# Performance work log

Measured on AMD Instinct MI355X. Metric: run time of the kernel, lower is better.

The kernel has to match this reference:

```python
import jax, jax.numpy as jnp
from jax import lax
import numpy as np

# Config mirroring init_kwargs
B, N, PD = 4, 16384, 3
PROJ = 64                 # projection_channel
M1, K1, C1 = 2048, 32, 128  # level-1 SA: fps points, neighbors, out channel
M2, K2, C2 = 512, 32, 256   # level-2 SA
DH, DO = 512, 256           # dense hidden / out (dense_channels)


def fps(pts, M):
    """Farthest point sampling. pts: [N,3] -> indices [M] (starts at point 0)."""
    n = pts.shape[0]
    def step(carry, _):
        dmin, last = carry
        d = jnp.sum((pts - pts[last]) ** 2, axis=-1)   # dist to newest center
        dmin = jnp.minimum(dmin, d)
        nxt = jnp.argmax(dmin).astype(jnp.int32)
        return (dmin, nxt), last
    init = (jnp.full((n,), 1e10, pts.dtype), jnp.int32(0))
    _, idxs = lax.scan(step, init, None, length=M)
    return idxs


def sa_level(pts, feats, M, K, Wa, ba, Wb, bb):
    """PointNet++ set abstraction: FPS + kNN (xyz space) + grouped MLP + max."""
    idx = jax.vmap(lambda p: fps(p, M))(pts)                       # [B,M]
    centers = jnp.take_along_axis(pts, idx[:, :, None], axis=1)    # [B,M,3]
    d = jnp.sum((centers[:, :, None, :] - pts[:, None, :, :]) ** 2, -1)  # [B,M,N]
    _, nidx = lax.top_k(-d, K)                                      # [B,M,K]
    gather = jax.vmap(lambda a, i: a[i])
    rel = gather(pts, nidx) - centers[:, :, None, :]                # [B,M,K,3]
    nf = gather(feats, nidx)                                        # [B,M,K,C]
    g = jnp.concatenate([rel, nf], axis=-1)                         # use_xyz=True
    h = jax.nn.relu(g @ Wa + ba)
    h = jax.nn.relu(h @ Wb + bb)
    return centers, jnp.max(h, axis=2)                              # [B,M,Cout]


def setup_inputs() -> dict:
    key = jax.random.key(0)
    ks = jax.random.split(key, 12)
    w = lambda k, shape, s: jax.random.normal(k, shape, jnp.float32) * s
    z = lambda c: jnp.zeros((c,), jnp.float32)
    return {
        "xyz": jax.random.normal(ks[0], (B, N, PD), jnp.float32),
        "Wp": w(ks[1], (PD, PROJ), 0.3), "bp": z(PROJ),
        "W1a": w(ks[2], (PROJ + 3, C1), 0.1), "b1a": z(C1),
        "W1b": w(ks[3], (C1, C1), 0.08), "b1b": z(C1),
        "W2a": w(ks[4], (C1 + 3, C2), 0.08), "b2a": z(C2),
        "W2b": w(ks[5], (C2, C2), 0.06), "b2b": z(C2),
        "Wd1": w(ks[6], (2 * C2, DH), 0.05), "bd1": z(DH),
        "Wd2": w(ks[7], (DH, DO), 0.05), "bd2": z(DO),
    }


def reference(xyz, Wp, bp, W1a, b1a, W1b, b1b, W2a, b2a, W2b, b2b,
              Wd1, bd1, Wd2, bd2):
    feats = xyz @ Wp + bp            # point_proj: [B,N,PROJ]
    pts = xyz[..., :3]
    pts, feats = sa_level(pts, feats, M1, K1, W1a, b1a, W1b, b1b)
    pts, feats = sa_level(pts, feats, M2, K2, W2a, b2a, W2b, b2b)
    # global max + avg pool (adaptive_max/avg_pool1d to 1), concat -> [B,2*C2]
    g = jnp.concatenate([jnp.max(feats, axis=1), jnp.mean(feats, axis=1)], -1)
    h = jax.nn.relu(g @ Wd1 + bd1)   # DenseBlock w/ activation
    return h @ Wd2 + bd2             # last block: no activation (last_activation=False)
```

## Files before the change

### kernel.cpp

```cpp
#include <hip/hip_runtime.h>

#define B_    4
#define N1_   16384
#define M1_   2048
#define M2_   512
#define KNN_  32
#define PROJ_ 64
#define C1_   128
#define C2_   256
#define PROJ_BLKS_ ((B_ * N1_ * PROJ_) / 512)
#define KNN_BLKS_  ((M1_ / 64) * (B_ * 64))

__device__ __forceinline__ float sqdist_exact(float px, float py, float pz,
                                              float cx, float cy, float cz) {
    float dx = __fsub_rn(px, cx);
    float dy = __fsub_rn(py, cy);
    float dz = __fsub_rn(pz, cz);
    return __fadd_rn(__fadd_rn(__fmul_rn(dx, dx), __fmul_rn(dy, dy)), __fmul_rn(dz, dz));
}

typedef float v2f __attribute__((ext_vector_type(2)));

template<int CTRL, int RM>
__device__ __forceinline__ unsigned long long dpp_umax64(unsigned long long pk) {
    unsigned lo = (unsigned)__builtin_amdgcn_update_dpp(
        0, (int)(unsigned)pk, CTRL, RM, 0xf, true);
    unsigned hi = (unsigned)__builtin_amdgcn_update_dpp(
        0, (int)(unsigned)(pk >> 32), CTRL, RM, 0xf, true);
    unsigned long long o = ((unsigned long long)hi << 32) | (unsigned long long)lo;
    return (o > pk) ? o : pk;
}

__device__ __forceinline__ unsigned long long wave_max_key(unsigned long long pk) {
    pk = dpp_umax64<0x111, 0xf>(pk);
    pk = dpp_umax64<0x112, 0xf>(pk);
    pk = dpp_umax64<0x114, 0xf>(pk);
    pk = dpp_umax64<0x118, 0xf>(pk);
    pk = dpp_umax64<0x142, 0xa>(pk);
    pk = dpp_umax64<0x143, 0xc>(pk);
    return pk;
}

__device__ __forceinline__ unsigned reduce8_widx(const unsigned long long* wk,
                                                 int lane) {
    unsigned long long k8 = wk[lane & 7];
    k8 = dpp_umax64<0x111, 0xf>(k8);
    k8 = dpp_umax64<0x112, 0xf>(k8);
    k8 = dpp_umax64<0x114, 0xf>(k8);
    unsigned lo = (unsigned)__builtin_amdgcn_readlane((int)(unsigned)k8, 7);
    return ~lo;
}

__device__ __forceinline__ unsigned reduce2_widx(const unsigned long long* wk,
                                                 int lane) {
    unsigned long long k2 = wk[lane & 1];
    k2 = dpp_umax64<0x111, 0xf>(k2);
    unsigned lo = (unsigned)__builtin_amdgcn_readlane((int)(unsigned)k2, 1);
    return ~lo;
}

template<int N>
__device__ void knn_body512(const float* __restrict__ P,
                            float cx, float cy, float cz,
                            int* __restrict__ out, char* arena) {
    constexpr int K = KNN_;
    constexpr int CAP = 224;
    const int t = threadIdx.x;
    const int lane = t & 63;
    const int w = t >> 6;

    int*      hist = (int*)arena;
    unsigned* eqk  = (unsigned*)(arena + 8192);
    int*      eqi  = (int*)(arena + 8192 + 896);
    int*      wsum = (int*)(arena + 8192 + 1792);
    int*      ctrl = (int*)(arena + 8192 + 1824);

    unsigned prefix = 0; int pbits = 0;
    unsigned Tlo = 0; unsigned long long Thi = 0x100000000ull;
    int L = 0, target = K, Cbin = N;

    for (int round = 0; round < 3; ++round) {
        const int bits  = (round < 2) ? 11 : 10;
        const int nbins = 1 << bits;
        const int shift = 32 - pbits - bits;
        for (int i = t; i < nbins; i += 512) hist[i] = 0;
        __syncthreads();
        for (int j = t; j < N; j += 512) {
            float d = sqdist_exact(P[j * 3], P[j * 3 + 1], P[j * 3 + 2], cx, cy, cz);
            unsigned key = __float_as_uint(d);
            if (key >= Tlo && (unsigned long long)key < Thi)
                atomicAdd(&hist[(key >> shift) & (nbins - 1)], 1);
        }
        __syncthreads();
        const int per = nbins / 512;
        int s = 0;
        for (int i = 0; i < per; ++i) s += hist[t * per + i];
        int cum = s;
        for (int off = 1; off < 64; off <<= 1) {
            int o = __shfl_up(cum, off);
            if (lane >= off) cum += o;
        }
        if (lane == 63) wsum[w] = cum;
        __syncthreads();
        int wpre = 0;
        for (int i = 0; i < w; ++i) wpre += wsum[i];
        cum += wpre;
        const int cumex = cum - s;
        if ((cumex < target) && (cum >= target)) {
            int acc = cumex;
            for (int i = 0; i < per; ++i) {
                int h = hist[t * per + i];
                if (acc + h >= target) { ctrl[2] = t * per + i; ctrl[3] = acc; ctrl[4] = h; break; }
                acc += h;
            }
        }
        __syncthreads();
        const int binsel = ctrl[2];
        const int Ladd   = ctrl[3];
        const int bincnt = ctrl[4];
        L += Ladd;
        target -= Ladd;
        prefix = (prefix << bits) | (unsigned)binsel;
        pbits += bits;
        Tlo = prefix << (32 - pbits);
        Thi = ((unsigned long long)prefix + 1ull) << (32 - pbits);
        Cbin = bincnt;
        __syncthreads();
        if (Cbin <= CAP) break;
    }

    if (t == 0) { ctrl[0] = 0; ctrl[1] = 0; }
    __syncthreads();

    if (Cbin <= CAP) {
        for (int j = t; j < N; j += 512) {
            float d = sqdist_exact(P[j * 3], P[j * 3 + 1], P[j * 3 + 2], cx, cy, cz);
            unsigned key = __float_as_uint(d);
            if (key < Tlo) {
                int p = atomicAdd(&ctrl[0], 1);
                out[p] = j;
            } else if ((unsigned long long)key < Thi) {
                int p = atomicAdd(&ctrl[1], 1);
                eqk[p] = key; eqi[p] = j;
            }
        }
        __syncthreads();
        const int E = ctrl[1];
        for (int e = t; e < E; e += 512) {
            unsigned ke = eqk[e]; int ie = eqi[e];
            int rank = 0;
            for (int f = 0; f < E; ++f) {
                unsigned kf = eqk[f]; int jf = eqi[f];
                rank += (kf < ke || (kf == ke && jf < ie)) ? 1 : 0;
            }
            if (rank < target) out[L + rank] = ie;
        }
    } else {
        if (t < 64) {
            int cnt = 0;
            for (int jb = 0; jb < N; jb += 64) {
                int j = jb + lane;
                float d = sqdist_exact(P[j * 3], P[j * 3 + 1], P[j * 3 + 2], cx, cy, cz);
                unsigned key = __float_as_uint(d);
                if (key < Tlo) {
                    int p = atomicAdd(&ctrl[0], 1);
                    out[p] = j;
                }
                bool eq = (key == Tlo);
                unsigned long long mb = __ballot(eq);
                int below = __popcll(mb & ((1ull << lane) - 1ull));
                if (eq && (cnt + below) < target) out[L + cnt + below] = j;
                cnt += (int)__popcll(mb);
            }
        }
    }
}

__global__ __attribute__((amdgpu_flat_work_group_size(512, 512)))
__attribute__((amdgpu_waves_per_eu(2, 2)))
void mega1_kernel(const float* __restrict__ xyz,
                  const float* __restrict__ Wp, const float* __restrict__ bp,
                  float* __restrict__ feats0, float* __restrict__ centers1,
                  int* __restrict__ nidx1, unsigned* __restrict__ prog) {
#pragma clang fp contract(off)
    __shared__ alignas(16) char arena[24832];
    asm volatile("" ::: "v255");
    const int bid = blockIdx.x;
    const int t = threadIdx.x;

    if (bid >= B_ + PROJ_BLKS_) {
        const int k = bid - (B_ + PROJ_BLKS_);
        const int c = k >> 8;
        const int b = (k >> 6) & 3;
        const int m = c * 64 + (k & 63);
        if (t == 0) {
            while (__hip_atomic_load(&prog[b * 16], __ATOMIC_RELAXED,
                                     __HIP_MEMORY_SCOPE_AGENT) <= (unsigned)c)
                __builtin_amdgcn_s_sleep(16);
        }
        __syncthreads();
        const unsigned* cw = (const unsigned*)(centers1 + ((size_t)b * M1_ + m) * 3);
        float cx = __uint_as_float(__hip_atomic_load(cw + 0, __ATOMIC_RELAXED, __HIP_MEMORY_SCOPE_AGENT));
        float cy = __uint_as_float(__hip_atomic_load(cw + 1, __ATOMIC_RELAXED, __HIP_MEMORY_SCOPE_AGENT));
        float cz = __uint_as_float(__hip_atomic_load(cw + 2, __ATOMIC_RELAXED, __HIP_MEMORY_SCOPE_AGENT));
        knn_body512<N1_>(xyz + (size_t)b * N1_ * 3, cx, cy, cz,
                         nidx1 + ((size_t)b * M1_ + m) * KNN_, arena);
        return;
    }
    if (bid >= B_) {
        int tid = (bid - B_) * 512 + t;
        int cc = tid & (PROJ_ - 1);
        int pn = tid >> 6;
        const float* p = xyz + (size_t)pn * 3;
        float acc = p[0] * Wp[0 * PROJ_ + cc];
        acc = __fmaf_rn(p[1], Wp[1 * PROJ_ + cc], acc);
        acc = __fmaf_rn(p[2], Wp[2 * PROJ_ + cc], acc);
        feats0[tid] = acc + bp[cc];
        return;
    }
    constexpr int NT = 512;
    constexpr int NW = NT / 64;
    constexpr int NP1 = (N1_ / NT) / 2;
    const int b = bid;
    const int w = t >> 6;
    const int lane = t & 63;
    const float* P = xyz + (size_t)b * N1_ * 3;
    float* C1 = centers1 + (size_t)b * M1_ * 3;

    unsigned long long (*wkey)[NW] = (unsigned long long(*)[NW])arena;
    float* cb1 = (float*)(arena + 128);

    v2f px2[NP1], py2[NP1], pz2[NP1];
    float dmin[2 * NP1];
#pragma unroll
    for (int p = 0; p < NP1; ++p) {
        const int j0 = (2 * p) * NT + t;
        const int j1 = j0 + NT;
        px2[p] = (v2f){P[j0 * 3 + 0], P[j1 * 3 + 0]};
        py2[p] = (v2f){P[j0 * 3 + 1], P[j1 * 3 + 1]};
        pz2[p] = (v2f){P[j0 * 3 + 2], P[j1 * 3 + 2]};
        dmin[2 * p] = 1e10f; dmin[2 * p + 1] = 1e10f;
    }
#pragma unroll
    for (int p = 0; p < NP1; ++p)
        asm volatile("" : "+v"(px2[p]), "+v"(py2[p]), "+v"(pz2[p]));

    float cx = P[0], cy = P[1], cz = P[2];

    for (int m = 0; m < M1_; ++m) {
        if (t == 0) {
            cb1[m * 3 + 0] = cx; cb1[m * 3 + 1] = cy; cb1[m * 3 + 2] = cz;
        }
        if ((m & 63) == 63) {
            __syncthreads();
            const int c = m >> 6;
            if (t < 48)
                ((float4*)C1)[c * 48 + t] = ((const float4*)cb1)[c * 48 + t];
            __syncthreads();
            if (t == 0)
                __hip_atomic_store(&prog[b * 16], (unsigned)(c + 1),
                                   __ATOMIC_RELEASE, __HIP_MEMORY_SCOPE_AGENT);
        }
        if (m == M1_ - 1) break;
        const int par = m & 1;
        const v2f c2x = {cx, cx}, c2y = {cy, cy}, c2z = {cz, cz};
        float bv = -1.0f; int bk = 0;
#pragma unroll
        for (int p = 0; p < NP1; ++p) {
            v2f dx = px2[p] - c2x;
            v2f dy = py2[p] - c2y;
            v2f dz = pz2[p] - c2z;
            v2f d2 = (dx * dx + dy * dy) + dz * dz;
            float nd0 = fminf(dmin[2 * p],     d2.x);
            float nd1 = fminf(dmin[2 * p + 1], d2.y);
            dmin[2 * p]     = nd0;
            dmin[2 * p + 1] = nd1;
            bool g0 = nd0 > bv; bv = g0 ? nd0 : bv; bk = g0 ? 2 * p     : bk;
            bool g1 = nd1 > bv; bv = g1 ? nd1 : bv; bk = g1 ? 2 * p + 1 : bk;
        }
        unsigned gi = (unsigned)(bk * NT + t);
        unsigned long long pk =
            ((unsigned long long)__float_as_uint(bv) << 32) | (unsigned)(~gi);
        pk = wave_max_key(pk);
        if (lane == 63) wkey[par][w] = pk;
        __syncthreads();
        const unsigned widx = reduce8_widx(wkey[par], lane);
        const float* cp = P + (size_t)widx * 3;
        cx = cp[0]; cy = cp[1]; cz = cp[2];
    }
}

__device__ __forceinline__ void fps2_body(const float* __restrict__ centers1,
                                          float* __restrict__ centers2,
                                          char* arena) {
#pragma clang fp contract(off)
    constexpr int NT = 128;
    constexpr int NW = 2;
    constexpr int NP = (M1_ / NT) / 2;
    const int b = blockIdx.x;
    const int t = threadIdx.x;
    const int w = t >> 6;
    const int lane = t & 63;
    const float* P = centers1 + (size_t)b * M1_ * 3;
    float* C = centers2 + (size_t)b * M2_ * 3;

    unsigned long long (*wkey)[NW] = (unsigned long long(*)[NW])arena;
    float* cb2 = (float*)(arena + 64);

    v2f px2[NP], py2[NP], pz2[NP];
    float dmin[2 * NP];
#pragma unroll
    for (int p = 0; p < NP; ++p) {
        const int j0 = (2 * p) * NT + t;
        const int j1 = j0 + NT;
        px2[p] = (v2f){P[j0 * 3 + 0], P[j1 * 3 + 0]};
        py2[p] = (v2f){P[j0 * 3 + 1], P[j1 * 3 + 1]};
        pz2[p] = (v2f){P[j0 * 3 + 2], P[j1 * 3 + 2]};
        dmin[2 * p] = 1e10f; dmin[2 * p + 1] = 1e10f;
    }
#pragma unroll
    for (int p = 0; p < NP; ++p)
        asm volatile("" : "+v"(px2[p]), "+v"(py2[p]), "+v"(pz2[p]));

    float cx = P[0], cy = P[1], cz = P[2];

    for (int m = 0; m < M2_; ++m) {
        if (t == 0) {
            cb2[m * 3 + 0] = cx; cb2[m * 3 + 1] = cy; cb2[m * 3 + 2] = cz;
        }
        if (m == M2_ - 1) break;
        const int par = m & 1;
        const v2f c2x = {cx, cx}, c2y = {cy, cy}, c2z = {cz, cz};
        float bv = -1.0f; int bk = 0;
#pragma unroll
        for (int p = 0; p < NP; ++p) {
            v2f dx = px2[p] - c2x;
            v2f dy = py2[p] - c2y;
            v2f dz = pz2[p] - c2z;
            v2f d2 = (dx * dx + dy * dy) + dz * dz;
            float nd0 = fminf(dmin[2 * p],     d2.x);
            float nd1 = fminf(dmin[2 * p + 1], d2.y);
            dmin[2 * p]     = nd0;
            dmin[2 * p + 1] = nd1;
            bool g0 = nd0 > bv; bv = g0 ? nd0 : bv; bk = g0 ? 2 * p     : bk;
            bool g1 = nd1 > bv; bv = g1 ? nd1 : bv; bk = g1 ? 2 * p + 1 : bk;
        }
        unsigned gi = (unsigned)(bk * NT + t);
        unsigned long long pk =
            ((unsigned long long)__float_as_uint(bv) << 32) | (unsigned)(~gi);
        pk = wave_max_key(pk);
        if (lane == 63) wkey[par][w] = pk;
        __syncthreads();
        const unsigned widx = reduce2_widx(wkey[par], lane);
        const float* cp = P + (size_t)widx * 3;
        cx = cp[0]; cy = cp[1]; cz = cp[2];
    }
    __syncthreads();
#pragma unroll 1
    for (int i = t; i < (M2_ * 3) / 4; i += NT)
        ((float4*)C)[i] = ((const float4*)cb2)[i];
}

template<int NPTS, int FD, int CO, int M>
__device__ __forceinline__ void mlp_body(int bm, char* arena,
                 const float* __restrict__ pts, const float* __restrict__ feats,
                 const float* __restrict__ centers, const int* __restrict__ nidx,
                 const float* __restrict__ Wa, const float* __restrict__ ba,
                 const float* __restrict__ Wb, const float* __restrict__ bb,
                 float* __restrict__ outf) {
    constexpr int KN = KNN_;
    constexpr int GS = FD + 4;
    const int b = bm / M;
    const int t = threadIdx.x;
    float (*g)[GS]  = (float(*)[GS])arena;
    float (*h1)[CO] = (float(*)[CO])(arena + sizeof(float) * KN * GS);
    const int* nb = nidx + (size_t)bm * KN;
    const float* cen = centers + (size_t)bm * 3;
    const float cx = cen[0], cy = cen[1], cz = cen[2];
    {
        constexpr int PARTS = CO / KN;
        constexpr int CHUNK = FD / PARTS;
        const int kk = t / PARTS;
        const int q  = t % PARTS;
        const int j  = nb[kk];
        const float* f = feats + ((size_t)b * NPTS + j) * FD + q * CHUNK;
        float* gr = &g[kk][q * CHUNK];
#pragma unroll
        for (int u = 0; u < CHUNK / 4; ++u)
            *(float4*)(gr + 4 * u) = *(const float4*)(f + 4 * u);
        if (q == 0) {
            const float* p = pts + ((size_t)b * NPTS + j) * 3;
            g[kk][FD + 0] = __fsub_rn(p[0], cx);
            g[kk][FD + 1] = __fsub_rn(p[1], cy);
            g[kk][FD + 2] = __fsub_rn(p[2], cz);
            g[kk][FD + 3] = 0.f;
        }
    }
    __syncthreads();
    const int o = t;
    float acc[KN];
#pragma unroll
    for (int k = 0; k < KN; ++k) acc[k] = ba[o];
    for (int s4 = 0; s4 < FD / 4; ++s4) {
        const float w0 = Wa[(4 * s4 + 3) * CO + o];
        const float w1 = Wa[(4 * s4 + 4) * CO + o];
        const float w2 = Wa[(4 * s4 + 5) * CO + o];
        const float w3 = Wa[(4 * s4 + 6) * CO + o];
#pragma unroll
        for (int k = 0; k < KN; ++k) {
            float4 gv = *(const float4*)&g[k][4 * s4];
            acc[k] = __fmaf_rn(gv.x, w0, acc[k]);
            acc[k] = __fmaf_rn(gv.y, w1, acc[k]);
            acc[k] = __fmaf_rn(gv.z, w2, acc[k]);
            acc[k] = __fmaf_rn(gv.w, w3, acc[k]);
        }
    }
    {
        const float w0 = Wa[0 * CO + o];
        const float w1 = Wa[1 * CO + o];
        const float w2 = Wa[2 * CO + o];
#pragma unroll
        for (int k = 0; k < KN; ++k) {
            float4 gv = *(const float4*)&g[k][FD];
            acc[k] = __fmaf_rn(gv.x, w0, acc[k]);
            acc[k] = __fmaf_rn(gv.y, w1, acc[k]);
            acc[k] = __fmaf_rn(gv.z, w2, acc[k]);
        }
    }
#pragma unroll
    for (int k = 0; k < KN; ++k) h1[k][o] = fmaxf(acc[k], 0.f);
    __syncthreads();
#pragma unroll
    for (int k = 0; k < KN; ++k) acc[k] = bb[o];
    for (int s4 = 0; s4 < CO / 4; ++s4) {
        const float w0 = Wb[(4 * s4 + 0) * CO + o];
        const float w1 = Wb[(4 * s4 + 1) * CO + o];
        const float w2 = Wb[(4 * s4 + 2) * CO + o];
        const float w3 = Wb[(4 * s4 + 3) * CO + o];
#pragma unroll
        for (int k = 0; k < KN; ++k) {
            float4 hv = *(const float4*)&h1[k][4 * s4];
            acc[k] = __fmaf_rn(hv.x, w0, acc[k]);
            acc[k] = __fmaf_rn(hv.y, w1, acc[k]);
            acc[k] = __fmaf_rn(hv.z, w2, acc[k]);
            acc[k] = __fmaf_rn(hv.w, w3, acc[k]);
        }
    }
    float mx = 0.f;
#pragma unroll
    for (int k = 0; k < KN; ++k) mx = fmaxf(mx, fmaxf(acc[k], 0.f));
    outf[(size_t)bm * CO + o] = mx;
}

__global__ void __launch_bounds__(C1_)
sa1_kernel(const float* __restrict__ xyz, const float* __restrict__ feats0,
           const float* __restrict__ centers1, const int* __restrict__ nidx1,
           const float* __restrict__ W1a, const float* __restrict__ b1a,
           const float* __restrict__ W1b, const float* __restrict__ b1b,
           float* __restrict__ feats1, float* __restrict__ centers2) {
    constexpr size_t MLP_BYTES =
        sizeof(float) * (KNN_ * (PROJ_ + 4) + KNN_ * C1_);
    __shared__ alignas(16) char arena[MLP_BYTES];
    if (blockIdx.x < B_) {
        fps2_body(centers1, centers2, arena);
        return;
    }
    mlp_body<N1_, PROJ_, C1_, M1_>(blockIdx.x - B_, arena, xyz, feats0,
                                   centers1, nidx1, W1a, b1a, W1b, b1b, feats1);
}

template<int NPTS, int FD, int CO, int M>
__global__ void __launch_bounds__(CO)
group_mlp_kernel(const float* __restrict__ pts, const float* __restrict__ feats,
                 const float* __restrict__ centers, const int* __restrict__ nidx,
                 const float* __restrict__ Wa, const float* __restrict__ ba,
                 const float* __restrict__ Wb, const float* __restrict__ bb,
                 float* __restrict__ outf) {
    constexpr size_t BYTES = sizeof(float) * (KNN_ * (FD + 4) + KNN_ * CO);
    __shared__ alignas(16) char arena[BYTES];
    mlp_body<NPTS, FD, CO, M>(blockIdx.x, arena, pts, feats, centers, nidx,
                              Wa, ba, Wb, bb, outf);
}

template<int N, int M>
__global__ void __launch_bounds__(64)
knn_kernel(const float* __restrict__ pts, const float* __restrict__ centers,
           int* __restrict__ nidx) {
    constexpr int K = KNN_;
    constexpr int CAP = 224;
    const int bm = blockIdx.x;
    const int b = bm / M;
    const int lane = threadIdx.x;
    const float* P = pts + (size_t)b * N * 3;
    const float* c = centers + (size_t)bm * 3;
    const float cx = c[0], cy = c[1], cz = c[2];
    int* out = nidx + (size_t)bm * K;

    __shared__ int hist[2048];
    __shared__ unsigned int eqk[CAP];
    __shared__ int eqi[CAP];
    __shared__ int cnt_less, cnt_eq;

    unsigned int prefix = 0; int pbits = 0;
    unsigned int Tlo = 0; unsigned long long Thi = 0x100000000ull;
    int L = 0, target = K, Cbin = N;

    for (int round = 0; round < 3; ++round) {
        const int bits  = (round < 2) ? 11 : 10;
        const int nbins = 1 << bits;
        const int shift = 32 - pbits - bits;
        for (int i = lane; i < nbins; i += 64) hist[i] = 0;
        __syncthreads();
        for (int j = lane; j < N; j += 64) {
            float d = sqdist_exact(P[j * 3], P[j * 3 + 1], P[j * 3 + 2], cx, cy, cz);
            unsigned int key = __float_as_uint(d);
            if (key >= Tlo && (unsigned long long)key < Thi)
                atomicAdd(&hist[(key >> shift) & (nbins - 1)], 1);
        }
        __syncthreads();
        const int per = nbins / 64;
        int s = 0;
        for (int i = 0; i < per; ++i) s += hist[lane * per + i];
        int cum = s;
        for (int off = 1; off < 64; off <<= 1) {
            int o = __shfl_up(cum, off);
            if (lane >= off) cum += o;
        }
        int cumex = cum - s;
        bool has = (cumex < target) && (cum >= target);
        unsigned long long ball = __ballot(has);
        int src = __ffsll(ball) - 1;
        int binsel = 0, Ladd = 0, bincnt = 0;
        if (lane == src) {
            int acc = cumex;
            for (int i = 0; i < per; ++i) {
                int h = hist[lane * per + i];
                if (acc + h >= target) { binsel = lane * per + i; Ladd = acc; bincnt = h; break; }
                acc += h;
            }
        }
        binsel = __shfl(binsel, src);
        Ladd   = __shfl(Ladd, src);
        bincnt = __shfl(bincnt, src);
        L += Ladd;
        target -= Ladd;
        prefix = (prefix << bits) | (unsigned int)binsel;
        pbits += bits;
        Tlo = prefix << (32 - pbits);
        Thi = ((unsigned long long)prefix + 1ull) << (32 - pbits);
        Cbin = bincnt;
        __syncthreads();
        if (Cbin <= CAP) break;
    }

    if (lane == 0) { cnt_less = 0; cnt_eq = 0; }
    __syncthreads();

    if (Cbin <= CAP) {
        for (int j = lane; j < N; j += 64) {
            float d = sqdist_exact(P[j * 3], P[j * 3 + 1], P[j * 3 + 2], cx, cy, cz);
            unsigned int key = __float_as_uint(d);
            if (key < Tlo) {
                int p = atomicAdd(&cnt_less, 1);
                out[p] = j;
            } else if ((unsigned long long)key < Thi) {
                int p = atomicAdd(&cnt_eq, 1);
                eqk[p] = key; eqi[p] = j;
            }
        }
        __syncthreads();
        const int E = cnt_eq;
        for (int e = lane; e < E; e += 64) {
            unsigned int ke = eqk[e]; int ie = eqi[e];
            int rank = 0;
            for (int f = 0; f < E; ++f) {
                unsigned int kf = eqk[f]; int jf = eqi[f];
                rank += (kf < ke || (kf == ke && jf < ie)) ? 1 : 0;
            }
            if (rank < target) out[L + rank] = ie;
        }
    } else {
        int cnt = 0;
        for (int jb = 0; jb < N; jb += 64) {
            int j = jb + lane;
            float d = sqdist_exact(P[j * 3], P[j * 3 + 1], P[j * 3 + 2], cx, cy, cz);
            unsigned int key = __float_as_uint(d);
            if (key < Tlo) {
                int p = atomicAdd(&cnt_less, 1);
                out[p] = j;
            }
            bool eq = (key == Tlo);
            unsigned long long mb = __ballot(eq);
            int below = __popcll(mb & ((1ull << lane) - 1ull));
            if (eq && (cnt + below) < target) out[L + cnt + below] = j;
            cnt += (int)__popcll(mb);
        }
    }
}

__global__ void __launch_bounds__(256)
head_kernel(const float* __restrict__ feats2,
            const float* __restrict__ Wd1, const float* __restrict__ bd1,
            const float* __restrict__ Wd2, const float* __restrict__ bd2,
            float* __restrict__ outp) {
    const int b = blockIdx.x, t = threadIdx.x;
    __shared__ float gsh[2 * C2_];
    __shared__ float hsh[512];
    const float* F = feats2 + (size_t)b * M2_ * C2_;
    float mx = -1e30f, sm = 0.f;
    for (int r = 0; r < M2_; ++r) {
        float v = F[r * C2_ + t];
        mx = fmaxf(mx, v);
        sm += v;
    }
    gsh[t] = mx;
    gsh[C2_ + t] = sm * (1.0f / (float)M2_);
    __syncthreads();
#pragma unroll
    for (int oo = 0; oo < 2; ++oo) {
        const int o = t + oo * 256;
        float acc = bd1[o];
        for (int i = 0; i < 512; ++i)
            acc = __fmaf_rn(gsh[i], Wd1[i * 512 + o], acc);
        hsh[o] = fmaxf(acc, 0.f);
    }
    __syncthreads();
    float acc = bd2[t];
    for (int i = 0; i < 512; ++i)
        acc = __fmaf_rn(hsh[i], Wd2[i * 256 + t], acc);
    outp[b * 256 + t] = acc;
}

extern "C" void kernel_launch(void* const* d_in, const int* in_sizes, int n_in,
                              void* d_out, int out_size, void* d_ws, size_t ws_size,
                              hipStream_t stream) {
    const float* xyz = (const float*)d_in[0];
    const float* Wp  = (const float*)d_in[1];
    const float* bp  = (const float*)d_in[2];
    const float* W1a = (const float*)d_in[3];
    const float* b1a = (const float*)d_in[4];
    const float* W1b = (const float*)d_in[5];
    const float* b1b = (const float*)d_in[6];
    const float* W2a = (const float*)d_in[7];
    const float* b2a = (const float*)d_in[8];
    const float* W2b = (const float*)d_in[9];
    const float* b2b = (const float*)d_in[10];
    const float* Wd1 = (const float*)d_in[11];
    const float* bd1 = (const float*)d_in[12];
    const float* Wd2 = (const float*)d_in[13];
    const float* bd2 = (const float*)d_in[14];
    float* out = (float*)d_out;

    char* ws = (char*)d_ws;
    size_t off = 0;
    auto alloc = [&](size_t bytes) { void* p = ws + off; off += (bytes + 255) & ~(size_t)255; return p; };
    float* feats0   = (float*)alloc((size_t)B_ * N1_ * PROJ_ * 4);
    float* centers1 = (float*)alloc((size_t)B_ * M1_ * 3 * 4);
    int*   nidx1    = (int*)  alloc((size_t)B_ * M1_ * KNN_ * 4);
    float* feats1   = (float*)alloc((size_t)B_ * M1_ * C1_ * 4);
    float* centers2 = (float*)alloc((size_t)B_ * M2_ * 3 * 4);
    int*   nidx2    = (int*)  alloc((size_t)B_ * M2_ * KNN_ * 4);
    float* feats2   = (float*)alloc((size_t)B_ * M2_ * C2_ * 4);
    unsigned* prog  = (unsigned*)alloc(B_ * 16 * 4);
    (void)in_sizes; (void)n_in; (void)out_size; (void)ws_size;

    hipMemsetAsync(prog, 0, B_ * 16 * 4, stream);

    mega1_kernel<<<dim3(B_ + PROJ_BLKS_ + KNN_BLKS_), dim3(512), 0, stream>>>(
        xyz, Wp, bp, feats0, centers1, nidx1, prog);
    sa1_kernel<<<dim3(B_ + B_ * M1_), dim3(C1_), 0, stream>>>(
        xyz, feats0, centers1, nidx1, W1a, b1a, W1b, b1b, feats1, centers2);
    knn_kernel<M1_, M2_><<<dim3(B_ * M2_), dim3(64), 0, stream>>>(centers1, centers2, nidx2);
    group_mlp_kernel<M1_, C1_, C2_, M2_><<<dim3(B_ * M2_), dim3(C2_), 0, stream>>>(
        centers1, feats1, centers2, nidx2, W2a, b2a, W2b, b2b, feats2);
    head_kernel<<<dim3(B_), dim3(256), 0, stream>>>(feats2, Wd1, bd1, Wd2, bd2, out);
}
```

Before: 3.858 ms.

## Bucket points by x so FPS waves skip updates via bounding-slab test

Adds a pre-pass kernel that counting-sorts each batch's points by the top bits of their x coordinate into SoA arrays, carrying original indices. Each thread in the level-1 FPS loop now owns a contiguous run of x-sorted points, and each wave keeps its x-range and current max key. Whenever the new center's x-distance to that range cannot lower the wave's maximum min-distance, the wave skips the distance update entirely. This trades an extra kernel launch, extra workspace, per-point index loads and a possibly less vectorised inner loop for fewer distance evaluations in the serial FPS loop. The 0.999 margin is meant to keep the skip decision safe despite rounding.

```diff
diff --git a/kernel.cpp b/kernel.cpp
--- a/kernel.cpp
+++ b/kernel.cpp
@@ -17,6 +17,47 @@
     float dy = __fsub_rn(py, cy);
     float dz = __fsub_rn(pz, cz);
     return __fadd_rn(__fadd_rn(__fmul_rn(dx, dx), __fmul_rn(dy, dy)), __fmul_rn(dz, dz));
+}
+
+__global__ void __launch_bounds__(1024)
+sortx_kernel(const float* __restrict__ xyz, float* __restrict__ sx,
+             float* __restrict__ sy, float* __restrict__ sz,
+             unsigned* __restrict__ scid) {
+    const int b = blockIdx.x, t = threadIdx.x;
+    const int lane = t & 63, w = t >> 6;
+    const float* P = xyz + (size_t)b * N1_ * 3;
+    __shared__ int hist[1024];
+    __shared__ int wsum[16];
+    hist[t] = 0;
+    __syncthreads();
+    for (int j = t; j < N1_; j += 1024) {
+        unsigned kb = __float_as_uint(P[j * 3]);
+        kb ^= (kb >> 31) ? 0xFFFFFFFFu : 0x80000000u;
+        atomicAdd(&hist[kb >> 22], 1);
+    }
+    __syncthreads();
+    int v = hist[t];
+    int cum = v;
+    for (int off = 1; off < 64; off <<= 1) {
+        int o = __shfl_up(cum, off);
+        if (lane >= off) cum += o;
+    }
+    if (lane == 63) wsum[w] = cum;
+    __syncthreads();
+    int wpre = 0;
+    for (int i = 0; i < w; ++i) wpre += wsum[i];
+    const int excl = cum - v + wpre;
+    __syncthreads();
+    hist[t] = excl;
+    __syncthreads();
+    for (int j = t; j < N1_; j += 1024) {
+        float x = P[j * 3], y = P[j * 3 + 1], z = P[j * 3 + 2];
+        unsigned kb = __float_as_uint(x);
+        kb ^= (kb >> 31) ? 0xFFFFFFFFu : 0x80000000u;
+        int pos = atomicAdd(&hist[kb >> 22], 1);
+        size_t o = (size_t)b * N1_ + pos;
+        sx[o] = x; sy[o] = y; sz[o] = z; scid[o] = ~(unsigned)j;
+    }
 }
 
 typedef float v2f __attribute__((ext_vector_type(2)));
@@ -179,6 +220,8 @@
 __global__ __attribute__((amdgpu_flat_work_group_size(512, 512)))
 __attribute__((amdgpu_waves_per_eu(2, 2)))
 void mega1_kernel(const float* __restrict__ xyz,
+                  const float* __restrict__ sx, const float* __restrict__ sy,
+                  const float* __restrict__ sz, const unsigned* __restrict__ scid,
                   const float* __restrict__ Wp, const float* __restrict__ bp,
                   float* __restrict__ feats0, float* __restrict__ centers1,
                   int* __restrict__ nidx1, unsigned* __restrict__ prog) {
@@ -220,31 +263,45 @@
     }
     constexpr int NT = 512;
     constexpr int NW = NT / 64;
-    constexpr int NP1 = (N1_ / NT) / 2;
+    constexpr int PPT = N1_ / NT;
     const int b = bid;
     const int w = t >> 6;
     const int lane = t & 63;
-    const float* P = xyz + (size_t)b * N1_ * 3;
+    const float* P  = xyz + (size_t)b * N1_ * 3;
+    const float* SX = sx + (size_t)b * N1_;
+    const float* SY = sy + (size_t)b * N1_;
+    const float* SZ = sz + (size_t)b * N1_;
+    const unsigned* SC = scid + (size_t)b * N1_;
     float* C1 = centers1 + (size_t)b * M1_ * 3;
+    const int base = t * PPT;
 
     unsigned long long (*wkey)[NW] = (unsigned long long(*)[NW])arena;
     float* cb1 = (float*)(arena + 128);
 
-    v2f px2[NP1], py2[NP1], pz2[NP1];
-    float dmin[2 * NP1];
-#pragma unroll
-    for (int p = 0; p < NP1; ++p) {
-        const int j0 = (2 * p) * NT + t;
-        const int j1 = j0 + NT;
-        px2[p] = (v2f){P[j0 * 3 + 0], P[j1 * 3 + 0]};
-        py2[p] = (v2f){P[j0 * 3 + 1], P[j1 * 3 + 1]};
-        pz2[p] = (v2f){P[j0 * 3 + 2], P[j1 * 3 + 2]};
-        dmin[2 * p] = 1e10f; dmin[2 * p + 1] = 1e10f;
-    }
-#pragma unroll
-    for (int p = 0; p < NP1; ++p)
-        asm volatile("" : "+v"(px2[p]), "+v"(py2[p]), "+v"(pz2[p]));
-
+    float px[PPT], py[PPT], pz[PPT], dmin[PPT];
+#pragma unroll
+    for (int k = 0; k < PPT; ++k) {
+        px[k] = SX[base + k];
+        py[k] = SY[base + k];
+        pz[k] = SZ[base + k];
+        dmin[k] = 1e10f;
+    }
+#pragma unroll
+    for (int k = 0; k < PPT; ++k)
+        asm volatile("" : "+v"(px[k]), "+v"(py[k]), "+v"(pz[k]), "+v"(dmin[k]));
+
+    float xlo = px[0], xhi = px[0];
+#pragma unroll
+    for (int k = 1; k < PPT; ++k) {
+        xlo = fminf(xlo, px[k]);
+        xhi = fmaxf(xhi, px[k]);
+    }
+    for (int off = 1; off < 64; off <<= 1) {
+        xlo = fminf(xlo, __shfl_xor(xlo, off));
+        xhi = fmaxf(xhi, __shfl_xor(xhi, off));
+    }
+
+    unsigned long long mykey = ((unsigned long long)__float_as_uint(1e10f) << 32);
     float cx = P[0], cy = P[1], cz = P[2];
 
     for (int m = 0; m < M1_; ++m) {
@@ -263,26 +320,25 @@
         }
         if (m == M1_ - 1) break;
         const int par = m & 1;
-        const v2f c2x = {cx, cx}, c2y = {cy, cy}, c2z = {cz, cz};
-        float bv = -1.0f; int bk = 0;
-#pragma unroll
-        for (int p = 0; p < NP1; ++p) {
-            v2f dx = px2[p] - c2x;
-            v2f dy = py2[p] - c2y;
-            v2f dz = pz2[p] - c2z;
-            v2f d2 = (dx * dx + dy * dy) + dz * dz;
-            float nd0 = fminf(dmin[2 * p],     d2.x);
-            float nd1 = fminf(dmin[2 * p + 1], d2.y);
-            dmin[2 * p]     = nd0;
-            dmin[2 * p + 1] = nd1;
-            bool g0 = nd0 > bv; bv = g0 ? nd0 : bv; bk = g0 ? 2 * p     : bk;
-            bool g1 = nd1 > bv; bv = g1 ? nd1 : bv; bk = g1 ? 2 * p + 1 : bk;
-        }
-        unsigned gi = (unsigned)(bk * NT + t);
-        unsigned long long pk =
-            ((unsigned long long)__float_as_uint(bv) << 32) | (unsigned)(~gi);
-        pk = wave_max_key(pk);
-        if (lane == 63) wkey[par][w] = pk;
+        const float UBval = __uint_as_float((unsigned)(mykey >> 32));
+        const float dxs = fmaxf(fmaxf(xlo - cx, cx - xhi), 0.0f);
+        if (!(0.999f * (dxs * dxs) >= UBval)) {
+            unsigned long long pk = 0;
+#pragma unroll
+            for (int k = 0; k < PPT; ++k) {
+                float d  = sqdist_exact(px[k], py[k], pz[k], cx, cy, cz);
+                float nd = fminf(dmin[k], d);
+                dmin[k] = nd;
+                unsigned long long kk =
+                    ((unsigned long long)__float_as_uint(nd) << 32) | SC[base + k];
+                pk = (kk > pk) ? kk : pk;
+            }
+            pk = wave_max_key(pk);
+            unsigned klo = (unsigned)__builtin_amdgcn_readlane((int)(unsigned)pk, 63);
+            unsigned khi = (unsigned)__builtin_amdgcn_readlane((int)(unsigned)(pk >> 32), 63);
+            mykey = ((unsigned long long)khi << 32) | klo;
+        }
+        if (lane == 63) wkey[par][w] = mykey;
         __syncthreads();
         const unsigned widx = reduce8_widx(wkey[par], lane);
         const float* cp = P + (size_t)widx * 3;
@@ -662,12 +718,17 @@
     int*   nidx2    = (int*)  alloc((size_t)B_ * M2_ * KNN_ * 4);
     float* feats2   = (float*)alloc((size_t)B_ * M2_ * C2_ * 4);
     unsigned* prog  = (unsigned*)alloc(B_ * 16 * 4);
+    float* sx       = (float*)alloc((size_t)B_ * N1_ * 4);
+    float* sy       = (float*)alloc((size_t)B_ * N1_ * 4);
+    float* sz       = (float*)alloc((size_t)B_ * N1_ * 4);
+    unsigned* scid  = (unsigned*)alloc((size_t)B_ * N1_ * 4);
     (void)in_sizes; (void)n_in; (void)out_size; (void)ws_size;
 
     hipMemsetAsync(prog, 0, B_ * 16 * 4, stream);
 
+    sortx_kernel<<<dim3(B_), dim3(1024), 0, stream>>>(xyz, sx, sy, sz, scid);
     mega1_kernel<<<dim3(B_ + PROJ_BLKS_ + KNN_BLKS_), dim3(512), 0, stream>>>(
-        xyz, Wp, bp, feats0, centers1, nidx1, prog);
+        xyz, sx, sy, sz, scid, Wp, bp, feats0, centers1, nidx1, prog);
     sa1_kernel<<<dim3(B_ + B_ * M1_), dim3(C1_), 0, stream>>>(
         xyz, feats0, centers1, nidx1, W1a, b1a, W1b, b1b, feats1, centers2);
     knn_kernel<M1_, M2_><<<dim3(B_ * M2_), dim3(64), 0, stream>>>(centers1, centers2, nidx2);
```

Result: faster. 3.768 ms (-2.3%).
